# Optimization experiments

Measured on AMD Instinct MI355X. Metric: run time of the kernel, lower is better.

## Reference

```python
import jax, jax.numpy as jnp
import numpy as np


def _det3x3(m):
    # faithful translation of batch_det_3x3 (column-expansion form)
    return (m[..., 0, 0] * m[..., 1, 1] * m[..., 2, 2]
            + m[..., 1, 0] * m[..., 2, 1] * m[..., 0, 2]
            + m[..., 2, 0] * m[..., 1, 2] * m[..., 0, 1]
            - m[..., 0, 2] * m[..., 1, 1] * m[..., 2, 0]
            - m[..., 1, 2] * m[..., 2, 1] * m[..., 0, 0]
            - m[..., 2, 2] * m[..., 1, 0] * m[..., 0, 1])


def setup_inputs() -> dict:
    key = jax.random.key(0)
    k1, k2 = jax.random.split(key)
    B, C = 32768, 256
    x = jax.random.normal(k1, (B, C, 3, 3), dtype=jnp.float32)
    W = jax.random.normal(k2, (C,), dtype=jnp.float32) * (1.0 / np.sqrt(C))
    return {"x": x, "W": W}


def reference(x, W):
    # 1x1 conv with single output channel, no bias -> contraction over C
    camera = jnp.einsum('bchw,c->bhw', x, W)  # [B, 3, 3]
    # SVD-based orthonormalization. torch.svd returns V with A = U S V^T;
    # jnp.linalg.svd returns Vh = V^T, so torch's u @ v.transpose == u @ vh.
    u, s, vh = jnp.linalg.svd(camera, full_matrices=False)
    orth = jnp.matmul(u, vh)  # [B, 3, 3]
    # reflection fix: flip last column of U by det(orth) (+-1), recompose
    det = _det3x3(orth)  # [B]
    u_flip = jnp.concatenate([u[..., :2], u[..., 2:3] * det[:, None, None]], axis=-1)
    return jnp.matmul(u_flip, vh)
```

## Files before the change

kernel.cpp:

```cpp
#include <hip/hip_runtime.h>

constexpr int WAVES_PER_BLOCK = 4;
constexpr int BS_PER_WAVE = 8;

__global__ __launch_bounds__(256) void camera_reduce_kernel(
    const float4* __restrict__ x4, const float* __restrict__ W,
    float* __restrict__ cam, int B)
{
    __shared__ float4 tile[WAVES_PER_BLOCK][576];
    const int wave = threadIdx.x >> 6;
    const int lane = threadIdx.x & 63;
    const int wave_id = blockIdx.x * WAVES_PER_BLOCK + wave;
    const float4 wv = reinterpret_cast<const float4*>(W)[lane];
    float4* my = tile[wave];

    const int b0 = wave_id * BS_PER_WAVE;
    for (int i = 0; i < BS_PER_WAVE; ++i) {
        const int b = b0 + i;
        if (b >= B) break;

        const float4* src = x4 + (size_t)b * 576 + lane;
        float4 r[9];
        #pragma unroll
        for (int k = 0; k < 9; ++k) r[k] = src[(size_t)k * 64];

        #pragma unroll
        for (int k = 0; k < 9; ++k) my[lane + 64 * k] = r[k];

        float a0 = 0.f, a1 = 0.f, a2 = 0.f, a3 = 0.f, a4 = 0.f,
              a5 = 0.f, a6 = 0.f, a7 = 0.f, a8 = 0.f;
        float4 v;
        v = my[9*lane+0]; a0 += v.x*wv.x; a1 += v.y*wv.x; a2 += v.z*wv.x; a3 += v.w*wv.x;
        v = my[9*lane+1]; a4 += v.x*wv.x; a5 += v.y*wv.x; a6 += v.z*wv.x; a7 += v.w*wv.x;
        v = my[9*lane+2]; a8 += v.x*wv.x; a0 += v.y*wv.y; a1 += v.z*wv.y; a2 += v.w*wv.y;
        v = my[9*lane+3]; a3 += v.x*wv.y; a4 += v.y*wv.y; a5 += v.z*wv.y; a6 += v.w*wv.y;
        v = my[9*lane+4]; a7 += v.x*wv.y; a8 += v.y*wv.y; a0 += v.z*wv.z; a1 += v.w*wv.z;
        v = my[9*lane+5]; a2 += v.x*wv.z; a3 += v.y*wv.z; a4 += v.z*wv.z; a5 += v.w*wv.z;
        v = my[9*lane+6]; a6 += v.x*wv.z; a7 += v.y*wv.z; a8 += v.z*wv.z; a0 += v.w*wv.w;
        v = my[9*lane+7]; a1 += v.x*wv.w; a2 += v.y*wv.w; a3 += v.z*wv.w; a4 += v.w*wv.w;
        v = my[9*lane+8]; a5 += v.x*wv.w; a6 += v.y*wv.w; a7 += v.z*wv.w; a8 += v.w*wv.w;

        #pragma unroll
        for (int m = 32; m >= 1; m >>= 1) {
            a0 += __shfl_xor(a0, m, 64);
            a1 += __shfl_xor(a1, m, 64);
            a2 += __shfl_xor(a2, m, 64);
            a3 += __shfl_xor(a3, m, 64);
            a4 += __shfl_xor(a4, m, 64);
            a5 += __shfl_xor(a5, m, 64);
            a6 += __shfl_xor(a6, m, 64);
            a7 += __shfl_xor(a7, m, 64);
            a8 += __shfl_xor(a8, m, 64);
        }

        if (lane < 9) {
            float out = (lane == 0) ? a0 : (lane == 1) ? a1 : (lane == 2) ? a2 :
                        (lane == 3) ? a3 : (lane == 4) ? a4 : (lane == 5) ? a5 :
                        (lane == 6) ? a6 : (lane == 7) ? a7 : a8;
            cam[(size_t)b * 9 + lane] = out;
        }
    }
}

#define JROT(P, Q)                                                         \
  do {                                                                     \
    float apq = A[P][Q];                                                   \
    if (fabsf(apq) > 1e-20f) {                                             \
      float app = A[P][P], aqq = A[Q][Q];                                  \
      float tau = (aqq - app) / (2.0f * apq);                              \
      float tt = copysignf(1.0f, tau) /                                    \
                 (fabsf(tau) + sqrtf(tau * tau + 1.0f));                   \
      float c = rsqrtf(tt * tt + 1.0f);                                    \
      float s = tt * c;                                                    \
      _Pragma("unroll") for (int k = 0; k < 4; ++k) {                      \
        float t1 = A[k][P], t2 = A[k][Q];                                  \
        A[k][P] = c * t1 - s * t2;                                         \
        A[k][Q] = s * t1 + c * t2;                                         \
      }                                                                    \
      _Pragma("unroll") for (int k = 0; k < 4; ++k) {                      \
        float t1 = A[P][k], t2 = A[Q][k];                                  \
        A[P][k] = c * t1 - s * t2;                                         \
        A[Q][k] = s * t1 + c * t2;                                         \
      }                                                                    \
      _Pragma("unroll") for (int k = 0; k < 4; ++k) {                      \
        float t1 = V[k][P], t2 = V[k][Q];                                  \
        V[k][P] = c * t1 - s * t2;                                         \
        V[k][Q] = s * t1 + c * t2;                                         \
      }                                                                    \
    }                                                                      \
  } while (0)

__global__ __launch_bounds__(256) void polar_so3_kernel(float* __restrict__ io,
                                                        int B)
{
    const int t = blockIdx.x * blockDim.x + threadIdx.x;
    if (t >= B) return;
    float* p = io + (size_t)t * 9;
    const float m00 = p[0], m01 = p[1], m02 = p[2];
    const float m10 = p[3], m11 = p[4], m12 = p[5];
    const float m20 = p[6], m21 = p[7], m22 = p[8];

    float A[4][4];
    A[0][0] = m00 + m11 + m22;
    A[1][1] = m00 - m11 - m22;
    A[2][2] = m11 - m00 - m22;
    A[3][3] = m22 - m00 - m11;
    A[0][1] = A[1][0] = m21 - m12;
    A[0][2] = A[2][0] = m02 - m20;
    A[0][3] = A[3][0] = m10 - m01;
    A[1][2] = A[2][1] = m01 + m10;
    A[1][3] = A[3][1] = m02 + m20;
    A[2][3] = A[3][2] = m12 + m21;

    float V[4][4] = {{1.f, 0.f, 0.f, 0.f},
                     {0.f, 1.f, 0.f, 0.f},
                     {0.f, 0.f, 1.f, 0.f},
                     {0.f, 0.f, 0.f, 1.f}};

    #pragma unroll
    for (int sweep = 0; sweep < 5; ++sweep) {
        JROT(0, 1); JROT(0, 2); JROT(0, 3);
        JROT(1, 2); JROT(1, 3); JROT(2, 3);
    }

    int best = 0;
    float bd = A[0][0];
    if (A[1][1] > bd) { bd = A[1][1]; best = 1; }
    if (A[2][2] > bd) { bd = A[2][2]; best = 2; }
    if (A[3][3] > bd) { bd = A[3][3]; best = 3; }
    float qw = (best == 0) ? V[0][0] : (best == 1) ? V[0][1] : (best == 2) ? V[0][2] : V[0][3];
    float qx = (best == 0) ? V[1][0] : (best == 1) ? V[1][1] : (best == 2) ? V[1][2] : V[1][3];
    float qy = (best == 0) ? V[2][0] : (best == 1) ? V[2][1] : (best == 2) ? V[2][2] : V[2][3];
    float qz = (best == 0) ? V[3][0] : (best == 1) ? V[3][1] : (best == 2) ? V[3][2] : V[3][3];

    const float nrm = rsqrtf(qw * qw + qx * qx + qy * qy + qz * qz);
    qw *= nrm; qx *= nrm; qy *= nrm; qz *= nrm;

    const float xx = qx * qx, yy = qy * qy, zz = qz * qz;
    const float xy = qx * qy, xz = qx * qz, yz = qy * qz;
    const float wx = qw * qx, wy = qw * qy, wz = qw * qz;

    p[0] = 1.0f - 2.0f * (yy + zz);
    p[1] = 2.0f * (xy - wz);
    p[2] = 2.0f * (xz + wy);
    p[3] = 2.0f * (xy + wz);
    p[4] = 1.0f - 2.0f * (xx + zz);
    p[5] = 2.0f * (yz - wx);
    p[6] = 2.0f * (xz - wy);
    p[7] = 2.0f * (yz + wx);
    p[8] = 1.0f - 2.0f * (xx + yy);
}

extern "C" void kernel_launch(void* const* d_in, const int* in_sizes, int n_in,
                              void* d_out, int out_size, void* d_ws, size_t ws_size,
                              hipStream_t stream)
{
    const float* x = (const float*)d_in[0];
    const float* W = (const float*)d_in[1];
    float* out = (float*)d_out;

    const int C = in_sizes[1];
    const int B = in_sizes[0] / (C * 9);

    const int waves_needed = (B + BS_PER_WAVE - 1) / BS_PER_WAVE;
    const int blocks = (waves_needed + WAVES_PER_BLOCK - 1) / WAVES_PER_BLOCK;

    camera_reduce_kernel<<<blocks, 256, 0, stream>>>(
        (const float4*)x, W, out, B);
    polar_so3_kernel<<<(B + 255) / 256, 256, 0, stream>>>(out, B);
}
```

Baseline: 411.7 us.

## Fuse camera reduction and polar SO3 orthonormalization into one kernel

Merges the channel-contraction kernel and the per-matrix Jacobi polar kernel into a single launch. Each wave keeps the 9 reduced values for its 8 batch items in registers, one lane per item, and runs the Jacobi step for those items directly, which removes the second launch and the intermediate round trip through global memory. Input loads become nontemporal and launch bounds request 4 blocks per CU. The cost is that only 8 of 64 lanes run the polar step in each wave, and that step's register use may lower occupancy of the bandwidth-bound loop.

```diff
diff --git a/kernel.cpp b/kernel.cpp
--- a/kernel.cpp
+++ b/kernel.cpp
@@ -1,66 +1,9 @@
 #include <hip/hip_runtime.h>
+
+typedef float vf4 __attribute__((ext_vector_type(4)));
 
 constexpr int WAVES_PER_BLOCK = 4;
 constexpr int BS_PER_WAVE = 8;
-
-__global__ __launch_bounds__(256) void camera_reduce_kernel(
-    const float4* __restrict__ x4, const float* __restrict__ W,
-    float* __restrict__ cam, int B)
-{
-    __shared__ float4 tile[WAVES_PER_BLOCK][576];
-    const int wave = threadIdx.x >> 6;
-    const int lane = threadIdx.x & 63;
-    const int wave_id = blockIdx.x * WAVES_PER_BLOCK + wave;
-    const float4 wv = reinterpret_cast<const float4*>(W)[lane];
-    float4* my = tile[wave];
-
-    const int b0 = wave_id * BS_PER_WAVE;
-    for (int i = 0; i < BS_PER_WAVE; ++i) {
-        const int b = b0 + i;
-        if (b >= B) break;
-
-        const float4* src = x4 + (size_t)b * 576 + lane;
-        float4 r[9];
-        #pragma unroll
-        for (int k = 0; k < 9; ++k) r[k] = src[(size_t)k * 64];
-
-        #pragma unroll
-        for (int k = 0; k < 9; ++k) my[lane + 64 * k] = r[k];
-
-        float a0 = 0.f, a1 = 0.f, a2 = 0.f, a3 = 0.f, a4 = 0.f,
-              a5 = 0.f, a6 = 0.f, a7 = 0.f, a8 = 0.f;
-        float4 v;
-        v = my[9*lane+0]; a0 += v.x*wv.x; a1 += v.y*wv.x; a2 += v.z*wv.x; a3 += v.w*wv.x;
-        v = my[9*lane+1]; a4 += v.x*wv.x; a5 += v.y*wv.x; a6 += v.z*wv.x; a7 += v.w*wv.x;
-        v = my[9*lane+2]; a8 += v.x*wv.x; a0 += v.y*wv.y; a1 += v.z*wv.y; a2 += v.w*wv.y;
-        v = my[9*lane+3]; a3 += v.x*wv.y; a4 += v.y*wv.y; a5 += v.z*wv.y; a6 += v.w*wv.y;
-        v = my[9*lane+4]; a7 += v.x*wv.y; a8 += v.y*wv.y; a0 += v.z*wv.z; a1 += v.w*wv.z;
-        v = my[9*lane+5]; a2 += v.x*wv.z; a3 += v.y*wv.z; a4 += v.z*wv.z; a5 += v.w*wv.z;
-        v = my[9*lane+6]; a6 += v.x*wv.z; a7 += v.y*wv.z; a8 += v.z*wv.z; a0 += v.w*wv.w;
-        v = my[9*lane+7]; a1 += v.x*wv.w; a2 += v.y*wv.w; a3 += v.z*wv.w; a4 += v.w*wv.w;
-        v = my[9*lane+8]; a5 += v.x*wv.w; a6 += v.y*wv.w; a7 += v.z*wv.w; a8 += v.w*wv.w;
-
-        #pragma unroll
-        for (int m = 32; m >= 1; m >>= 1) {
-            a0 += __shfl_xor(a0, m, 64);
-            a1 += __shfl_xor(a1, m, 64);
-            a2 += __shfl_xor(a2, m, 64);
-            a3 += __shfl_xor(a3, m, 64);
-            a4 += __shfl_xor(a4, m, 64);
-            a5 += __shfl_xor(a5, m, 64);
-            a6 += __shfl_xor(a6, m, 64);
-            a7 += __shfl_xor(a7, m, 64);
-            a8 += __shfl_xor(a8, m, 64);
-        }
-
-        if (lane < 9) {
-            float out = (lane == 0) ? a0 : (lane == 1) ? a1 : (lane == 2) ? a2 :
-                        (lane == 3) ? a3 : (lane == 4) ? a4 : (lane == 5) ? a5 :
-                        (lane == 6) ? a6 : (lane == 7) ? a7 : a8;
-            cam[(size_t)b * 9 + lane] = out;
-        }
-    }
-}
 
 #define JROT(P, Q)                                                         \
   do {                                                                     \
@@ -90,27 +33,19 @@
     }                                                                      \
   } while (0)
 
-__global__ __launch_bounds__(256) void polar_so3_kernel(float* __restrict__ io,
-                                                        int B)
+__device__ __forceinline__ void polar_so3(const float m[9], float* __restrict__ p)
 {
-    const int t = blockIdx.x * blockDim.x + threadIdx.x;
-    if (t >= B) return;
-    float* p = io + (size_t)t * 9;
-    const float m00 = p[0], m01 = p[1], m02 = p[2];
-    const float m10 = p[3], m11 = p[4], m12 = p[5];
-    const float m20 = p[6], m21 = p[7], m22 = p[8];
-
     float A[4][4];
-    A[0][0] = m00 + m11 + m22;
-    A[1][1] = m00 - m11 - m22;
-    A[2][2] = m11 - m00 - m22;
-    A[3][3] = m22 - m00 - m11;
-    A[0][1] = A[1][0] = m21 - m12;
-    A[0][2] = A[2][0] = m02 - m20;
-    A[0][3] = A[3][0] = m10 - m01;
-    A[1][2] = A[2][1] = m01 + m10;
-    A[1][3] = A[3][1] = m02 + m20;
-    A[2][3] = A[3][2] = m12 + m21;
+    A[0][0] = m[0] + m[4] + m[8];
+    A[1][1] = m[0] - m[4] - m[8];
+    A[2][2] = m[4] - m[0] - m[8];
+    A[3][3] = m[8] - m[0] - m[4];
+    A[0][1] = A[1][0] = m[7] - m[5];
+    A[0][2] = A[2][0] = m[2] - m[6];
+    A[0][3] = A[3][0] = m[3] - m[1];
+    A[1][2] = A[2][1] = m[1] + m[3];
+    A[1][3] = A[3][1] = m[2] + m[6];
+    A[2][3] = A[3][2] = m[5] + m[7];
 
     float V[4][4] = {{1.f, 0.f, 0.f, 0.f},
                      {0.f, 1.f, 0.f, 0.f},
@@ -151,6 +86,71 @@
     p[8] = 1.0f - 2.0f * (xx + yy);
 }
 
+__global__ __launch_bounds__(256, 4) void camera_orth_kernel(
+    const vf4* __restrict__ x4, const float* __restrict__ W,
+    float* __restrict__ out, int B)
+{
+    __shared__ vf4 tile[WAVES_PER_BLOCK][576];
+    const int wave = threadIdx.x >> 6;
+    const int lane = threadIdx.x & 63;
+    const int b0 = (blockIdx.x * WAVES_PER_BLOCK + wave) * BS_PER_WAVE;
+    const vf4 wv = reinterpret_cast<const vf4*>(W)[lane];
+    vf4* my = tile[wave];
+
+    float cam[9];
+
+    for (int i = 0; i < BS_PER_WAVE; ++i) {
+        const int b = b0 + i;
+        if (b >= B) break;
+
+        const vf4* src = x4 + (size_t)b * 576 + lane;
+        vf4 r[9];
+        #pragma unroll
+        for (int k = 0; k < 9; ++k)
+            r[k] = __builtin_nontemporal_load(src + (size_t)k * 64);
+
+        #pragma unroll
+        for (int k = 0; k < 9; ++k) my[lane + 64 * k] = r[k];
+
+        float a0 = 0.f, a1 = 0.f, a2 = 0.f, a3 = 0.f, a4 = 0.f,
+              a5 = 0.f, a6 = 0.f, a7 = 0.f, a8 = 0.f;
+        vf4 v;
+        v = my[9*lane+0]; a0 += v.x*wv.x; a1 += v.y*wv.x; a2 += v.z*wv.x; a3 += v.w*wv.x;
+        v = my[9*lane+1]; a4 += v.x*wv.x; a5 += v.y*wv.x; a6 += v.z*wv.x; a7 += v.w*wv.x;
+        v = my[9*lane+2]; a8 += v.x*wv.x; a0 += v.y*wv.y; a1 += v.z*wv.y; a2 += v.w*wv.y;
+        v = my[9*lane+3]; a3 += v.x*wv.y; a4 += v.y*wv.y; a5 += v.z*wv.y; a6 += v.w*wv.y;
+        v = my[9*lane+4]; a7 += v.x*wv.y; a8 += v.y*wv.y; a0 += v.z*wv.z; a1 += v.w*wv.z;
+        v = my[9*lane+5]; a2 += v.x*wv.z; a3 += v.y*wv.z; a4 += v.z*wv.z; a5 += v.w*wv.z;
+        v = my[9*lane+6]; a6 += v.x*wv.z; a7 += v.y*wv.z; a8 += v.z*wv.z; a0 += v.w*wv.w;
+        v = my[9*lane+7]; a1 += v.x*wv.w; a2 += v.y*wv.w; a3 += v.z*wv.w; a4 += v.w*wv.w;
+        v = my[9*lane+8]; a5 += v.x*wv.w; a6 += v.y*wv.w; a7 += v.z*wv.w; a8 += v.w*wv.w;
+
+        #pragma unroll
+        for (int m = 32; m >= 1; m >>= 1) {
+            a0 += __shfl_xor(a0, m, 64);
+            a1 += __shfl_xor(a1, m, 64);
+            a2 += __shfl_xor(a2, m, 64);
+            a3 += __shfl_xor(a3, m, 64);
+            a4 += __shfl_xor(a4, m, 64);
+            a5 += __shfl_xor(a5, m, 64);
+            a6 += __shfl_xor(a6, m, 64);
+            a7 += __shfl_xor(a7, m, 64);
+            a8 += __shfl_xor(a8, m, 64);
+        }
+
+        if (lane == i) {
+            cam[0] = a0; cam[1] = a1; cam[2] = a2;
+            cam[3] = a3; cam[4] = a4; cam[5] = a5;
+            cam[6] = a6; cam[7] = a7; cam[8] = a8;
+        }
+    }
+
+    const int b = b0 + lane;
+    if (lane < BS_PER_WAVE && b < B) {
+        polar_so3(cam, out + (size_t)b * 9);
+    }
+}
+
 extern "C" void kernel_launch(void* const* d_in, const int* in_sizes, int n_in,
                               void* d_out, int out_size, void* d_ws, size_t ws_size,
                               hipStream_t stream)
@@ -165,7 +165,6 @@
     const int waves_needed = (B + BS_PER_WAVE - 1) / BS_PER_WAVE;
     const int blocks = (waves_needed + WAVES_PER_BLOCK - 1) / WAVES_PER_BLOCK;
 
-    camera_reduce_kernel<<<blocks, 256, 0, stream>>>(
-        (const float4*)x, W, out, B);
-    polar_so3_kernel<<<(B + 255) / 256, 256, 0, stream>>>(out, B);
+    camera_orth_kernel<<<blocks, 256, 0, stream>>>(
+        (const vf4*)x, W, out, B);
 }
```

New measurement: 416.6 us. About the same (+1.2%).
